# Kernel tuning notes

Measured on AMD Instinct MI355X. Metric: run time of the kernel, lower is better.

Reference implementation:

```python
import jax, jax.numpy as jnp
import numpy as np

N = 65536   # num rois (batch*num_rois)
C = 512     # input_channels
D = 512     # output_dims = num_heads * head_dims
H = 8       # num_heads
HD = 64     # head_dims
L = 16      # hardcoded expand size in forward
BN_EPS = 1e-5


def _bn(x, gamma, beta, mean, var):
    # eval-mode BatchNorm1d over channel axis 1 of [N, D, L]
    inv = gamma / jnp.sqrt(var + BN_EPS)
    return x * inv[None, :, None] + (beta - mean * inv)[None, :, None]


def setup_inputs() -> dict:
    key = jax.random.key(0)
    ks = jax.random.split(key, 12)
    w = lambda k, shape: jax.random.normal(k, shape, jnp.float32) * 0.05
    return {
        "features": jax.random.normal(ks[0], (N, C), jnp.float32),
        "features2": jax.random.normal(ks[1], (N, C), jnp.float32),
        "Wk": w(ks[2], (D, C)),      # key_proj conv1d weight (shared for pos & key)
        "Wv1": w(ks[3], (D, C)),     # value_proj conv1d #1
        "Wv2": w(ks[4], (D, D)),     # value_proj conv1d #2
        "bn1_gamma": jnp.ones((D,), jnp.float32),
        "bn1_beta": jnp.zeros((D,), jnp.float32),
        "bn1_mean": jax.random.normal(ks[5], (D,), jnp.float32) * 0.1,
        "bn1_var": jax.random.uniform(ks[6], (D,), jnp.float32, 0.5, 1.5),
        "bn2_gamma": jnp.ones((D,), jnp.float32),
        "bn2_beta": jnp.zeros((D,), jnp.float32),
        "bn2_mean": jax.random.normal(ks[7], (D,), jnp.float32) * 0.1,
        "bn2_var": jax.random.uniform(ks[8], (D,), jnp.float32, 0.5, 1.5),
        "Wa": w(ks[9], (H, D)),      # attention_proj conv1d
        "Wqk": w(ks[10], (D, D)),    # qk_coef Linear
        "Wvc": w(ks[11], (D, D)),    # v_coef Linear
    }


def reference(features, features2, Wk, Wv1, Wv2,
              bn1_gamma, bn1_beta, bn1_mean, bn1_var,
              bn2_gamma, bn2_beta, bn2_mean, bn2_var,
              Wa, Wqk, Wvc):
    # expand [N, C] -> [N, C, L] (all L columns identical, as in torch .expand)
    f = jnp.broadcast_to(features[:, :, None], (features.shape[0], features.shape[1], L))
    f2 = jnp.broadcast_to(features2[:, :, None], (features2.shape[0], features2.shape[1], L))

    # key_proj (shared weights) on both inputs: 1x1 conv + ReLU
    pos = jax.nn.relu(jnp.einsum('oc,ncl->nol', Wk, f))
    key_e = jax.nn.relu(jnp.einsum('oc,ncl->nol', Wk, f2))

    # value_proj: conv -> BN -> ReLU -> conv -> BN -> ReLU
    h = jax.nn.relu(_bn(jnp.einsum('oc,ncl->nol', Wv1, f2), bn1_gamma, bn1_beta, bn1_mean, bn1_var))
    value = jax.nn.relu(_bn(jnp.einsum('od,ndl->nol', Wv2, h), bn2_gamma, bn2_beta, bn2_mean, bn2_var))

    pk = pos * key_e                                    # [N, D, L]
    v_coef = jax.nn.sigmoid(pos.mean(axis=2) @ Wvc.T)   # [N, D]
    qk_coef = jax.nn.sigmoid(pk.mean(axis=2) @ Wqk.T)   # [N, D]

    value = value + pos * v_coef[:, :, None]
    attn_emb = pk * qk_coef[:, :, None]

    attn = jnp.einsum('hd,ndl->nhl', Wa, attn_emb)      # [N, H, L]
    attn = jax.nn.softmax(attn, axis=-1)
    attn = jnp.repeat(attn, HD, axis=1)                 # [N, H*HD, L], head-major

    return jnp.sum(attn * value, axis=-1)               # [N, D]
```

## Files before the change

kernel.cpp:

```cpp
#include <hip/hip_runtime.h>
#include <hip/hip_bf16.h>
#include <cstdint>
#include <cstddef>

#define DIM 512
#define NROWS 65536

typedef __bf16 bf16;
typedef __attribute__((ext_vector_type(8))) __bf16 bf16x8;
typedef __attribute__((ext_vector_type(4))) __bf16 bf16x4;
typedef __attribute__((ext_vector_type(4))) float f32x4;

__device__ __forceinline__ void async_copy16(const void* g, void* l) {
  __builtin_amdgcn_global_load_lds(
      (const __attribute__((address_space(1))) void*)g,
      (__attribute__((address_space(3))) void*)l, 16, 0, 0);
}

__device__ __forceinline__ float sigmoidf_(float x) {
  return 1.0f / (1.0f + __expf(-x));
}

__global__ __launch_bounds__(256) void cvt_f32_bf16(
    const float* __restrict__ s, bf16* __restrict__ d, int n4) {
  int i = blockIdx.x * 256 + threadIdx.x;
  if (i < n4) {
    f32x4 v = ((const f32x4*)s)[i];
    bf16x4 o;
    o[0] = (bf16)v[0]; o[1] = (bf16)v[1]; o[2] = (bf16)v[2]; o[3] = (bf16)v[3];
    ((bf16x4*)d)[i] = o;
  }
}

template <int EPI, bool AF32, typename OutT>
__global__ __launch_bounds__(256) void gemm_ep(
    const void* __restrict__ Av, const bf16* __restrict__ W,
    OutT* __restrict__ Out, const bf16* __restrict__ Extra,
    const float* __restrict__ bn_g, const float* __restrict__ bn_b,
    const float* __restrict__ bn_m, const float* __restrict__ bn_v) {
  __shared__ __align__(16) char AsmRaw[AF32 ? 128 * 32 * 4 : 128 * 32 * 2];
  __shared__ __align__(16) bf16 Bsm[128 * 32];

  const int t = threadIdx.x;
  const int lane = t & 63;
  const int wv = t >> 6;
  const int wm = (wv & 1) * 64;
  const int wn = (wv >> 1) * 64;
  const int lr = lane & 15;
  const int kq = lane >> 4;

  const int m0 = blockIdx.y * 128;
  const int n0 = blockIdx.x * 128;

  const bf16* gB = W + (size_t)(n0 + (t >> 2)) * DIM + (t & 3) * 8;
  bf16* lB = &Bsm[t * 8];

  const float* gAf = nullptr; const bf16* gAh = nullptr;
  float* lAf = nullptr; bf16* lAh = nullptr;
  if constexpr (AF32) {
    gAf = (const float*)Av + (size_t)(m0 + (t >> 3)) * DIM + (t & 7) * 4;
    lAf = (float*)AsmRaw + t * 4;
  } else {
    gAh = (const bf16*)Av + (size_t)(m0 + (t >> 2)) * DIM + (t & 3) * 8;
    lAh = (bf16*)AsmRaw + t * 8;
  }

  f32x4 acc[4][4];
#pragma unroll
  for (int i = 0; i < 4; i++)
#pragma unroll
    for (int j = 0; j < 4; j++) acc[i][j] = (f32x4){0.f, 0.f, 0.f, 0.f};

  for (int kb = 0; kb < DIM; kb += 32) {
    if constexpr (AF32) {
      async_copy16(gAf + kb, lAf);
      async_copy16(gAf + kb + (size_t)32 * DIM, lAf + 1024);
      async_copy16(gAf + kb + (size_t)64 * DIM, lAf + 2048);
      async_copy16(gAf + kb + (size_t)96 * DIM, lAf + 3072);
    } else {
      async_copy16(gAh + kb, lAh);
      async_copy16(gAh + kb + (size_t)64 * DIM, lAh + 64 * 32);
    }
    async_copy16(gB + kb, lB);
    async_copy16(gB + kb + (size_t)64 * DIM, lB + 64 * 32);
    __syncthreads();

    bf16x8 af[4], bfr[4];
#pragma unroll
    for (int i = 0; i < 4; i++) {
      if constexpr (AF32) {
        const float* p = (const float*)AsmRaw + (wm + i * 16 + lr) * 32 + kq * 8;
        f32x4 lo = *(const f32x4*)p;
        f32x4 hi = *(const f32x4*)(p + 4);
        bf16x8 a;
        a[0] = (bf16)lo[0]; a[1] = (bf16)lo[1];
        a[2] = (bf16)lo[2]; a[3] = (bf16)lo[3];
        a[4] = (bf16)hi[0]; a[5] = (bf16)hi[1];
        a[6] = (bf16)hi[2]; a[7] = (bf16)hi[3];
        af[i] = a;
      } else {
        af[i] = *(const bf16x8*)((const bf16*)AsmRaw +
                                 (wm + i * 16 + lr) * 32 + kq * 8);
      }
      bfr[i] = *(const bf16x8*)&Bsm[(wn + i * 16 + lr) * 32 + kq * 8];
    }
#pragma unroll
    for (int i = 0; i < 4; i++)
#pragma unroll
      for (int j = 0; j < 4; j++)
        acc[i][j] = __builtin_amdgcn_mfma_f32_16x16x32_bf16(af[i], bfr[j],
                                                            acc[i][j], 0, 0, 0);
    __syncthreads();
  }

  float invj[4], bbj[4];
  if (EPI >= 2) {
#pragma unroll
    for (int j = 0; j < 4; j++) {
      int c = n0 + wn + j * 16 + lr;
      float iv = bn_g[c] * rsqrtf(bn_v[c] + 1e-5f);
      invj[j] = iv;
      bbj[j] = bn_b[c] - bn_m[c] * iv;
    }
  }
#pragma unroll
  for (int i = 0; i < 4; i++) {
#pragma unroll
    for (int r = 0; r < 4; r++) {
      size_t row = (size_t)(m0 + wm + i * 16 + kq * 4 + r) * DIM;
#pragma unroll
      for (int j = 0; j < 4; j++) {
        int c = n0 + wn + j * 16 + lr;
        float v = acc[i][j][r];
        if (EPI == 0) {
          v = fmaxf(v, 0.f);
        } else if (EPI == 1) {
          v = sigmoidf_(v) * (float)Extra[row + c];
        } else {
          v = fmaxf(v * invj[j] + bbj[j], 0.f);
          if (EPI == 3) v += (float)Extra[row + c];
        }
        Out[row + c] = (OutT)v;
      }
    }
  }
}

extern "C" void kernel_launch(void* const* d_in, const int* in_sizes, int n_in,
                              void* d_out, int out_size, void* d_ws,
                              size_t ws_size, hipStream_t stream) {
  const float* features  = (const float*)d_in[0];
  const float* features2 = (const float*)d_in[1];
  const float* Wk  = (const float*)d_in[2];
  const float* Wv1 = (const float*)d_in[3];
  const float* Wv2 = (const float*)d_in[4];
  const float* g1 = (const float*)d_in[5];
  const float* b1 = (const float*)d_in[6];
  const float* m1 = (const float*)d_in[7];
  const float* v1 = (const float*)d_in[8];
  const float* g2 = (const float*)d_in[9];
  const float* b2 = (const float*)d_in[10];
  const float* m2 = (const float*)d_in[11];
  const float* v2 = (const float*)d_in[12];
  const float* Wvc = (const float*)d_in[15];
  float* out = (float*)d_out;

  bf16* pos = (bf16*)d_ws;
  bf16* pv  = pos + (size_t)NROWS * DIM;
  bf16* wkb  = pv + (size_t)NROWS * DIM;
  bf16* wv1b = wkb + DIM * DIM;
  bf16* wv2b = wv1b + DIM * DIM;
  bf16* wvcb = wv2b + DIM * DIM;

  {
    int n4 = DIM * DIM / 4;
    dim3 cg(n4 / 256), cb(256);
    cvt_f32_bf16<<<cg, cb, 0, stream>>>(Wk, wkb, n4);
    cvt_f32_bf16<<<cg, cb, 0, stream>>>(Wv1, wv1b, n4);
    cvt_f32_bf16<<<cg, cb, 0, stream>>>(Wv2, wv2b, n4);
    cvt_f32_bf16<<<cg, cb, 0, stream>>>(Wvc, wvcb, n4);
  }

  dim3 grid(DIM / 128, NROWS / 128);
  dim3 block(256);

  gemm_ep<0, true, bf16><<<grid, block, 0, stream>>>(
      features, wkb, pos, nullptr, nullptr, nullptr, nullptr, nullptr);
  gemm_ep<1, false, bf16><<<grid, block, 0, stream>>>(
      pos, wvcb, pv, pos, nullptr, nullptr, nullptr, nullptr);
  gemm_ep<2, true, bf16><<<grid, block, 0, stream>>>(
      features2, wv1b, pos, nullptr, g1, b1, m1, v1);
  gemm_ep<3, false, float><<<grid, block, 0, stream>>>(
      pos, wv2b, out, pv, g2, b2, m2, v2);
}
```

Baseline: 590.3 us.

## Register-prefetch double-buffered GEMM loop, fuse value/coef GEMMs, swizzle blocks

Replaces the direct global-to-LDS async copies with a register-staged, double-buffered LDS pipeline. It prefetches two k-tiles ahead and converts fp32 A to bf16 before the LDS write, which halves LDS footprint and read traffic for fp32 inputs. The v_coef GEMM and the final Wv2 GEMM are fused into one kernel so the pv intermediate is never written or re-read. A 1D grid swizzle maps neighbouring blocks across XCDs, and the four weight conversions are merged into one launch. The cost is more registers, since the fused kernel keeps a second accumulator set live, which may reduce occupancy.

```diff
diff --git a/kernel.cpp b/kernel.cpp
--- a/kernel.cpp
+++ b/kernel.cpp
@@ -5,42 +5,28 @@
 
 #define DIM 512
 #define NROWS 65536
+#define NKT 16
 
 typedef __bf16 bf16;
 typedef __attribute__((ext_vector_type(8))) __bf16 bf16x8;
 typedef __attribute__((ext_vector_type(4))) __bf16 bf16x4;
 typedef __attribute__((ext_vector_type(4))) float f32x4;
 
-__device__ __forceinline__ void async_copy16(const void* g, void* l) {
-  __builtin_amdgcn_global_load_lds(
-      (const __attribute__((address_space(1))) void*)g,
-      (__attribute__((address_space(3))) void*)l, 16, 0, 0);
-}
-
 __device__ __forceinline__ float sigmoidf_(float x) {
   return 1.0f / (1.0f + __expf(-x));
 }
 
-__global__ __launch_bounds__(256) void cvt_f32_bf16(
-    const float* __restrict__ s, bf16* __restrict__ d, int n4) {
-  int i = blockIdx.x * 256 + threadIdx.x;
-  if (i < n4) {
-    f32x4 v = ((const f32x4*)s)[i];
-    bf16x4 o;
-    o[0] = (bf16)v[0]; o[1] = (bf16)v[1]; o[2] = (bf16)v[2]; o[3] = (bf16)v[3];
-    ((bf16x4*)d)[i] = o;
-  }
-}
-
-template <int EPI, bool AF32, typename OutT>
-__global__ __launch_bounds__(256) void gemm_ep(
-    const void* __restrict__ Av, const bf16* __restrict__ W,
-    OutT* __restrict__ Out, const bf16* __restrict__ Extra,
-    const float* __restrict__ bn_g, const float* __restrict__ bn_b,
-    const float* __restrict__ bn_m, const float* __restrict__ bn_v) {
-  __shared__ __align__(16) char AsmRaw[AF32 ? 128 * 32 * 4 : 128 * 32 * 2];
-  __shared__ __align__(16) bf16 Bsm[128 * 32];
-
+__device__ __forceinline__ void swizzle(int id, int& m0, int& n0) {
+  int xcd = id & 7;
+  int q = id >> 3;
+  m0 = ((q >> 2) * 8 + xcd) * 128;
+  n0 = (q & 3) * 128;
+}
+
+template <bool AF32>
+__device__ __forceinline__ void gemm_loop(
+    const void* __restrict__ Av, const bf16* __restrict__ W, int m0, int n0,
+    bf16* AsmB, bf16* BsmB, f32x4 (&acc)[4][4]) {
   const int t = threadIdx.x;
   const int lane = t & 63;
   const int wv = t >> 6;
@@ -49,72 +35,107 @@
   const int lr = lane & 15;
   const int kq = lane >> 4;
 
-  const int m0 = blockIdx.y * 128;
-  const int n0 = blockIdx.x * 128;
-
-  const bf16* gB = W + (size_t)(n0 + (t >> 2)) * DIM + (t & 3) * 8;
-  bf16* lB = &Bsm[t * 8];
-
-  const float* gAf = nullptr; const bf16* gAh = nullptr;
-  float* lAf = nullptr; bf16* lAh = nullptr;
-  if constexpr (AF32) {
-    gAf = (const float*)Av + (size_t)(m0 + (t >> 3)) * DIM + (t & 7) * 4;
-    lAf = (float*)AsmRaw + t * 4;
-  } else {
-    gAh = (const bf16*)Av + (size_t)(m0 + (t >> 2)) * DIM + (t & 3) * 8;
-    lAh = (bf16*)AsmRaw + t * 8;
-  }
+  const int ra = t >> 1;
+  const int ca = (t & 1) * 16;
+  const float* gAf = nullptr;
+  const bf16* gAh = nullptr;
+  if constexpr (AF32)
+    gAf = (const float*)Av + (size_t)(m0 + ra) * DIM + ca;
+  else
+    gAh = (const bf16*)Av + (size_t)(m0 + ra) * DIM + ca;
+  const bf16* gB = W + (size_t)(n0 + ra) * DIM + ca;
+  const int lofs = ra * 32 + ca;
+
+  f32x4 aF[2][4];
+  bf16x8 aH[2][2];
+  bf16x8 bR[2][2];
+
+  auto load_t = [&](int kt, int s) {
+    const int kb = kt * 32;
+    if constexpr (AF32) {
+      const f32x4* p = (const f32x4*)(gAf + kb);
+      aF[s][0] = p[0]; aF[s][1] = p[1]; aF[s][2] = p[2]; aF[s][3] = p[3];
+    } else {
+      const bf16x8* p = (const bf16x8*)(gAh + kb);
+      aH[s][0] = p[0]; aH[s][1] = p[1];
+    }
+    const bf16x8* pb = (const bf16x8*)(gB + kb);
+    bR[s][0] = pb[0]; bR[s][1] = pb[1];
+  };
+  auto write_t = [&](int buf, int s) {
+    bf16* la = AsmB + buf * (128 * 32) + lofs;
+    if constexpr (AF32) {
+      bf16x8 w0, w1;
+#pragma unroll
+      for (int j = 0; j < 4; j++) {
+        w0[j] = (bf16)aF[s][0][j]; w0[j + 4] = (bf16)aF[s][1][j];
+        w1[j] = (bf16)aF[s][2][j]; w1[j + 4] = (bf16)aF[s][3][j];
+      }
+      *(bf16x8*)la = w0; *(bf16x8*)(la + 8) = w1;
+    } else {
+      *(bf16x8*)la = aH[s][0]; *(bf16x8*)(la + 8) = aH[s][1];
+    }
+    bf16* lb = BsmB + buf * (128 * 32) + lofs;
+    *(bf16x8*)lb = bR[s][0]; *(bf16x8*)(lb + 8) = bR[s][1];
+  };
+
+  load_t(0, 0);
+  write_t(0, 0);
+  load_t(1, 1);
+  __syncthreads();
+
+  for (int k = 0; k < NKT; k++) {
+    const int p = k & 1;
+    if (k + 2 < NKT) load_t(k + 2, k & 1);
+
+    bf16x8 af[4], bf_[4];
+#pragma unroll
+    for (int i = 0; i < 4; i++) {
+      af[i]  = *(const bf16x8*)(AsmB + p * (128 * 32) + (wm + i * 16 + lr) * 32 + kq * 8);
+      bf_[i] = *(const bf16x8*)(BsmB + p * (128 * 32) + (wn + i * 16 + lr) * 32 + kq * 8);
+    }
+#pragma unroll
+    for (int i = 0; i < 4; i++)
+#pragma unroll
+      for (int j = 0; j < 4; j++)
+        acc[i][j] = __builtin_amdgcn_mfma_f32_16x16x32_bf16(af[i], bf_[j],
+                                                            acc[i][j], 0, 0, 0);
+    if (k + 1 < NKT) {
+      write_t(p ^ 1, (k + 1) & 1);
+      __syncthreads();
+    }
+  }
+}
+
+__device__ __forceinline__ void zero_acc(f32x4 (&acc)[4][4]) {
+#pragma unroll
+  for (int i = 0; i < 4; i++)
+#pragma unroll
+    for (int j = 0; j < 4; j++) acc[i][j] = (f32x4){0.f, 0.f, 0.f, 0.f};
+}
+
+template <int EPI>
+__global__ __launch_bounds__(256) void gemm_k13(
+    const float* __restrict__ A, const bf16* __restrict__ W,
+    bf16* __restrict__ Out, const float* __restrict__ bn_g,
+    const float* __restrict__ bn_b, const float* __restrict__ bn_m,
+    const float* __restrict__ bn_v) {
+  __shared__ bf16 Asm[2 * 128 * 32];
+  __shared__ bf16 Bsm[2 * 128 * 32];
+  int m0, n0;
+  swizzle(blockIdx.x, m0, n0);
 
   f32x4 acc[4][4];
-#pragma unroll
-  for (int i = 0; i < 4; i++)
-#pragma unroll
-    for (int j = 0; j < 4; j++) acc[i][j] = (f32x4){0.f, 0.f, 0.f, 0.f};
-
-  for (int kb = 0; kb < DIM; kb += 32) {
-    if constexpr (AF32) {
-      async_copy16(gAf + kb, lAf);
-      async_copy16(gAf + kb + (size_t)32 * DIM, lAf + 1024);
-      async_copy16(gAf + kb + (size_t)64 * DIM, lAf + 2048);
-      async_copy16(gAf + kb + (size_t)96 * DIM, lAf + 3072);
-    } else {
-      async_copy16(gAh + kb, lAh);
-      async_copy16(gAh + kb + (size_t)64 * DIM, lAh + 64 * 32);
-    }
-    async_copy16(gB + kb, lB);
-    async_copy16(gB + kb + (size_t)64 * DIM, lB + 64 * 32);
-    __syncthreads();
-
-    bf16x8 af[4], bfr[4];
-#pragma unroll
-    for (int i = 0; i < 4; i++) {
-      if constexpr (AF32) {
-        const float* p = (const float*)AsmRaw + (wm + i * 16 + lr) * 32 + kq * 8;
-        f32x4 lo = *(const f32x4*)p;
-        f32x4 hi = *(const f32x4*)(p + 4);
-        bf16x8 a;
-        a[0] = (bf16)lo[0]; a[1] = (bf16)lo[1];
-        a[2] = (bf16)lo[2]; a[3] = (bf16)lo[3];
-        a[4] = (bf16)hi[0]; a[5] = (bf16)hi[1];
-        a[6] = (bf16)hi[2]; a[7] = (bf16)hi[3];
-        af[i] = a;
-      } else {
-        af[i] = *(const bf16x8*)((const bf16*)AsmRaw +
-                                 (wm + i * 16 + lr) * 32 + kq * 8);
-      }
-      bfr[i] = *(const bf16x8*)&Bsm[(wn + i * 16 + lr) * 32 + kq * 8];
-    }
-#pragma unroll
-    for (int i = 0; i < 4; i++)
-#pragma unroll
-      for (int j = 0; j < 4; j++)
-        acc[i][j] = __builtin_amdgcn_mfma_f32_16x16x32_bf16(af[i], bfr[j],
-                                                            acc[i][j], 0, 0, 0);
-    __syncthreads();
-  }
+  zero_acc(acc);
+  gemm_loop<true>(A, W, m0, n0, Asm, Bsm, acc);
+
+  const int lane = threadIdx.x & 63;
+  const int wv = threadIdx.x >> 6;
+  const int wm = (wv & 1) * 64, wn = (wv >> 1) * 64;
+  const int lr = lane & 15, kq = lane >> 4;
 
   float invj[4], bbj[4];
-  if (EPI >= 2) {
+  if (EPI == 2) {
 #pragma unroll
     for (int j = 0; j < 4; j++) {
       int c = n0 + wn + j * 16 + lr;
@@ -132,18 +153,78 @@
       for (int j = 0; j < 4; j++) {
         int c = n0 + wn + j * 16 + lr;
         float v = acc[i][j][r];
-        if (EPI == 0) {
-          v = fmaxf(v, 0.f);
-        } else if (EPI == 1) {
-          v = sigmoidf_(v) * (float)Extra[row + c];
-        } else {
-          v = fmaxf(v * invj[j] + bbj[j], 0.f);
-          if (EPI == 3) v += (float)Extra[row + c];
-        }
-        Out[row + c] = (OutT)v;
+        if (EPI == 0) v = fmaxf(v, 0.f);
+        else          v = fmaxf(v * invj[j] + bbj[j], 0.f);
+        Out[row + c] = (bf16)v;
       }
     }
   }
+}
+
+__global__ __launch_bounds__(256) void gemm_fused(
+    const bf16* __restrict__ hmid, const bf16* __restrict__ pos,
+    const bf16* __restrict__ Wv2b, const bf16* __restrict__ Wvcb,
+    float* __restrict__ Out, const float* __restrict__ g2,
+    const float* __restrict__ b2, const float* __restrict__ m2,
+    const float* __restrict__ v2) {
+  __shared__ bf16 Asm[2 * 128 * 32];
+  __shared__ bf16 Bsm[2 * 128 * 32];
+  int m0, n0;
+  swizzle(blockIdx.x, m0, n0);
+
+  const int lane = threadIdx.x & 63;
+  const int wv = threadIdx.x >> 6;
+  const int wm = (wv & 1) * 64, wn = (wv >> 1) * 64;
+  const int lr = lane & 15, kq = lane >> 4;
+
+  f32x4 acc[4][4];
+  zero_acc(acc);
+  gemm_loop<false>(hmid, Wv2b, m0, n0, Asm, Bsm, acc);
+
+  f32x4 vout[4][4];
+#pragma unroll
+  for (int j = 0; j < 4; j++) {
+    int c = n0 + wn + j * 16 + lr;
+    float iv = g2[c] * rsqrtf(v2[c] + 1e-5f);
+    float bb = b2[c] - m2[c] * iv;
+#pragma unroll
+    for (int i = 0; i < 4; i++)
+#pragma unroll
+      for (int r = 0; r < 4; r++)
+        vout[i][j][r] = fmaxf(acc[i][j][r] * iv + bb, 0.f);
+  }
+
+  zero_acc(acc);
+  gemm_loop<false>(pos, Wvcb, m0, n0, Asm, Bsm, acc);
+
+#pragma unroll
+  for (int i = 0; i < 4; i++) {
+#pragma unroll
+    for (int r = 0; r < 4; r++) {
+      size_t row = (size_t)(m0 + wm + i * 16 + kq * 4 + r) * DIM;
+#pragma unroll
+      for (int j = 0; j < 4; j++) {
+        int c = n0 + wn + j * 16 + lr;
+        float pv = sigmoidf_(acc[i][j][r]) * (float)pos[row + c];
+        Out[row + c] = vout[i][j][r] + pv;
+      }
+    }
+  }
+}
+
+__global__ __launch_bounds__(256) void cvt_w(
+    const float* __restrict__ s0, const float* __restrict__ s1,
+    const float* __restrict__ s2, const float* __restrict__ s3,
+    bf16* __restrict__ d0, bf16* __restrict__ d1, bf16* __restrict__ d2,
+    bf16* __restrict__ d3) {
+  int w = blockIdx.x >> 8;
+  int i = (blockIdx.x & 255) * 256 + threadIdx.x;
+  const float* s = w == 0 ? s0 : w == 1 ? s1 : w == 2 ? s2 : s3;
+  bf16* d = w == 0 ? d0 : w == 1 ? d1 : w == 2 ? d2 : d3;
+  f32x4 v = ((const f32x4*)s)[i];
+  bf16x4 o;
+  o[0] = (bf16)v[0]; o[1] = (bf16)v[1]; o[2] = (bf16)v[2]; o[3] = (bf16)v[3];
+  ((bf16x4*)d)[i] = o;
 }
 
 extern "C" void kernel_launch(void* const* d_in, const int* in_sizes, int n_in,
@@ -165,31 +246,18 @@
   const float* Wvc = (const float*)d_in[15];
   float* out = (float*)d_out;
 
-  bf16* pos = (bf16*)d_ws;
-  bf16* pv  = pos + (size_t)NROWS * DIM;
-  bf16* wkb  = pv + (size_t)NROWS * DIM;
+  bf16* pos  = (bf16*)d_ws;
+  bf16* hmid = pos + (size_t)NROWS * DIM;
+  bf16* wkb  = hmid + (size_t)NROWS * DIM;
   bf16* wv1b = wkb + DIM * DIM;
   bf16* wv2b = wv1b + DIM * DIM;
   bf16* wvcb = wv2b + DIM * DIM;
 
-  {
-    int n4 = DIM * DIM / 4;
-    dim3 cg(n4 / 256), cb(256);
-    cvt_f32_bf16<<<cg, cb, 0, stream>>>(Wk, wkb, n4);
-    cvt_f32_bf16<<<cg, cb, 0, stream>>>(Wv1, wv1b, n4);
-    cvt_f32_bf16<<<cg, cb, 0, stream>>>(Wv2, wv2b, n4);
-    cvt_f32_bf16<<<cg, cb, 0, stream>>>(Wvc, wvcb, n4);
-  }
-
-  dim3 grid(DIM / 128, NROWS / 128);
-  dim3 block(256);
-
-  gemm_ep<0, true, bf16><<<grid, block, 0, stream>>>(
-      features, wkb, pos, nullptr, nullptr, nullptr, nullptr, nullptr);
-  gemm_ep<1, false, bf16><<<grid, block, 0, stream>>>(
-      pos, wvcb, pv, pos, nullptr, nullptr, nullptr, nullptr);
-  gemm_ep<2, true, bf16><<<grid, block, 0, stream>>>(
-      features2, wv1b, pos, nullptr, g1, b1, m1, v1);
-  gemm_ep<3, false, float><<<grid, block, 0, stream>>>(
-      pos, wv2b, out, pv, g2, b2, m2, v2);
-}
+  cvt_w<<<1024, 256, 0, stream>>>(Wk, Wv1, Wv2, Wvc, wkb, wv1b, wv2b, wvcb);
+
+  gemm_k13<0><<<2048, 256, 0, stream>>>(features, wkb, pos,
+                                        nullptr, nullptr, nullptr, nullptr);
+  gemm_k13<2><<<2048, 256, 0, stream>>>(features2, wv1b, hmid, g1, b1, m1, v1);
+  gemm_fused<<<2048, 256, 0, stream>>>(hmid, pos, wv2b, wvcb, out,
+                                       g2, b2, m2, v2);
+}
```

New measurement: 2.232 ms. 278% more time.
